# Kernel tuning notes

Hardware: AMD Instinct MI355X
Metric: run time of the kernel (lower is better)

The kernel has to match this reference:

```python
import jax, jax.numpy as jnp
import numpy as np

N = 100000      # num_nodes
E = 1600000     # num_edges (avg degree 16)
IN = 128        # in_channels
HID = 8         # hidden_channels (per head)
HEADS = 8
OUT = 64        # out_channels
NEG_SLOPE = 0.2


def setup_inputs() -> dict:
    key = jax.random.key(0)
    ks = jax.random.split(key, 11)
    s = 0.05
    return {
        "x": jax.random.normal(ks[0], (N, IN), jnp.float32),
        "edge_index": jax.random.randint(ks[1], (2, E), 0, N, dtype=jnp.int32),
        "W1": jax.random.normal(ks[2], (IN, HEADS * HID), jnp.float32) * s,
        "a_src1": jax.random.normal(ks[3], (HEADS, HID), jnp.float32) * s,
        "a_dst1": jax.random.normal(ks[4], (HEADS, HID), jnp.float32) * s,
        "b1": jnp.zeros((HEADS * HID,), jnp.float32),
        "W2": jax.random.normal(ks[5], (HEADS * HID, OUT), jnp.float32) * s,
        "a_src2": jax.random.normal(ks[6], (1, OUT), jnp.float32) * s,
        "a_dst2": jax.random.normal(ks[7], (1, OUT), jnp.float32) * s,
        "b2": jnp.zeros((OUT,), jnp.float32),
    }


def gat_conv(x, src, dst, W, a_src, a_dst, bias, heads, out_ch):
    """PyG GATConv (concat=True, dropout=0, self-loops already in src/dst)."""
    n = x.shape[0]
    h = (x @ W).reshape(n, heads, out_ch)               # [N, H, C]
    al_src = jnp.einsum('nhc,hc->nh', h, a_src)          # [N, H]
    al_dst = jnp.einsum('nhc,hc->nh', h, a_dst)          # [N, H]
    e = jax.nn.leaky_relu(al_src[src] + al_dst[dst], NEG_SLOPE)  # [E, H]
    # segment softmax over destination nodes (numerically stable)
    e_max = jax.ops.segment_max(e, dst, num_segments=n)  # [N, H]
    ex = jnp.exp(e - e_max[dst])
    denom = jax.ops.segment_sum(ex, dst, num_segments=n)
    alpha = ex / (denom[dst] + 1e-16)                    # [E, H]
    msg = h[src] * alpha[:, :, None]                     # [E, H, C]
    out = jax.ops.segment_sum(msg, dst, num_segments=n)  # [N, H, C]
    return out.reshape(n, heads * out_ch) + bias


def reference(x, edge_index, W1, a_src1, a_dst1, b1, W2, a_src2, a_dst2, b2):
    n = x.shape[0]
    loops = jnp.arange(n, dtype=edge_index.dtype)
    src = jnp.concatenate([edge_index[0], loops])        # add self-loops (PyG default)
    dst = jnp.concatenate([edge_index[1], loops])
    h = gat_conv(x, src, dst, W1, a_src1, a_dst1, b1, HEADS, HID)
    h = jax.nn.elu(h)
    out = gat_conv(h, src, dst, W2, a_src2, a_dst2, b2, 1, OUT)
    return out
```

## Files before the change

### kernel.cpp

```cpp
#include <hip/hip_runtime.h>
#include <hip/hip_bf16.h>

#define IN_CH   128
#define HEADS   8
#define HID     8
#define MID_CH  64
#define OUT_CH  64
#define CAP     64
#define NRANGE  8

typedef unsigned short u16;
__device__ __forceinline__ u16 f2bu(float f) {
    union { float f; unsigned int i; } v; v.f = f;
    unsigned int lsb = (v.i >> 16) & 1u;
    return (u16)((v.i + 0x7fffu + lsb) >> 16);
}
__device__ __forceinline__ float2 up2(unsigned int u) {
    union { unsigned int i; float f; } a, b;
    a.i = u << 16; b.i = u & 0xffff0000u;
    return make_float2(a.f, b.f);
}
__device__ __forceinline__ float lrelu(float e) { return (e > 0.f) ? e : 0.2f * e; }

#define FILL_ISSUE(U, D4, S4, P4)                                              \
    do {                                                                        \
        int range_ = (U) & (NRANGE - 1);                                        \
        int chunk_ = (U) >> 3;                                                  \
        int lo_ = (int)(((long long)N * range_) >> 3);                          \
        int hi_ = (int)(((long long)N * (range_ + 1)) >> 3);                    \
        int base_ = (chunk_ * 256 + threadIdx.x) * 4;                           \
        if (base_ + 3 < E) {                                                    \
            D4 = *(const int4*)(dst + base_);                                   \
            bool ix_ = (D4.x >= lo_ && D4.x < hi_);                             \
            bool iy_ = (D4.y >= lo_ && D4.y < hi_);                             \
            bool iz_ = (D4.z >= lo_ && D4.z < hi_);                             \
            bool iw_ = (D4.w >= lo_ && D4.w < hi_);                             \
            if (ix_ | iy_ | iz_ | iw_) {                                        \
                S4 = *(const int4*)(src + base_);                               \
                if (ix_) P4.x = atomicAdd(&deg[D4.x], 1);                       \
                if (iy_) P4.y = atomicAdd(&deg[D4.y], 1);                       \
                if (iz_) P4.z = atomicAdd(&deg[D4.z], 1);                       \
                if (iw_) P4.w = atomicAdd(&deg[D4.w], 1);                       \
            }                                                                   \
        } else {                                                                \
            for (int j_ = 0; j_ < 4; j_++) {                                    \
                int e_ = base_ + j_;                                            \
                if (e_ < E) {                                                   \
                    int d_ = dst[e_];                                           \
                    if (d_ >= lo_ && d_ < hi_) {                                \
                        int p_ = atomicAdd(&deg[d_], 1);                        \
                        if (p_ < CAP) adj[(size_t)d_ * CAP + p_] = src[e_];     \
                    }                                                           \
                }                                                               \
            }                                                                   \
        }                                                                       \
    } while (0)

#define FILL_STORE(D4, S4, P4)                                                  \
    do {                                                                        \
        if (P4.x < CAP) adj[(size_t)D4.x * CAP + P4.x] = S4.x;                  \
        if (P4.y < CAP) adj[(size_t)D4.y * CAP + P4.y] = S4.y;                  \
        if (P4.z < CAP) adj[(size_t)D4.z * CAP + P4.z] = S4.z;                  \
        if (P4.w < CAP) adj[(size_t)D4.w * CAP + P4.w] = S4.w;                  \
    } while (0)

__global__ __launch_bounds__(256, 4) void k12_fillgemm(
    const int* __restrict__ src, const int* __restrict__ dst,
    int* __restrict__ deg, int* __restrict__ adj,
    const float* __restrict__ x, const float* __restrict__ W1,
    const float* __restrict__ a_src, const float* __restrict__ a_dst,
    u16* __restrict__ h1b, float* __restrict__ als, float* __restrict__ ald,
    int E, int N, int grid, int nUnits)
{
    __shared__ float Wl[IN_CH * MID_CH];
    __shared__ float xl[16 * IN_CH];
    int tid = threadIdx.x;
    int bid = blockIdx.x;

    int4 dA = make_int4(0, 0, 0, 0), sA = make_int4(0, 0, 0, 0);
    int4 pA = make_int4(CAP, CAP, CAP, CAP);
    int4 dB = make_int4(0, 0, 0, 0), sB = make_int4(0, 0, 0, 0);
    int4 pB = make_int4(CAP, CAP, CAP, CAP);
    int uA = bid;
    int uB = bid + grid;
    if (uA < nUnits) FILL_ISSUE(uA, dA, sA, pA);
    if (uB < nUnits) FILL_ISSUE(uB, dB, sB, pB);

    {
        const float4* W4 = (const float4*)W1;
        float4* Wl4 = (float4*)Wl;
        #pragma unroll
        for (int i = tid; i < IN_CH * MID_CH / 4; i += 256) Wl4[i] = W4[i];
    }
    int base = bid * 16;
    {
        float4* xl4 = (float4*)xl;
        const float4* x4 = (const float4*)x;
        #pragma unroll
        for (int i = tid; i < 16 * IN_CH / 4; i += 256) {
            int r = i >> 5;
            int n = base + r;
            xl4[i] = (n < N) ? x4[(size_t)n * (IN_CH / 4) + (i & 31)]
                             : make_float4(0.f, 0.f, 0.f, 0.f);
        }
    }

    FILL_STORE(dA, sA, pA);
    FILL_STORE(dB, sB, pB);
    __syncthreads();

    int wave = tid >> 6, lane = tid & 63;
    int r0 = wave * 4;
    const float* xr0 = &xl[(r0 + 0) * IN_CH];
    const float* xr1 = &xl[(r0 + 1) * IN_CH];
    const float* xr2 = &xl[(r0 + 2) * IN_CH];
    const float* xr3 = &xl[(r0 + 3) * IN_CH];
    float acc0 = 0.f, acc1 = 0.f, acc2 = 0.f, acc3 = 0.f;
    #pragma unroll 8
    for (int kc = 0; kc < IN_CH; kc += 4) {
        float4 xa = *(const float4*)(xr0 + kc);
        float4 xb = *(const float4*)(xr1 + kc);
        float4 xc = *(const float4*)(xr2 + kc);
        float4 xd = *(const float4*)(xr3 + kc);
        float w0 = Wl[(kc + 0) * MID_CH + lane];
        float w1 = Wl[(kc + 1) * MID_CH + lane];
        float w2 = Wl[(kc + 2) * MID_CH + lane];
        float w3 = Wl[(kc + 3) * MID_CH + lane];
        acc0 = fmaf(xa.x, w0, acc0); acc0 = fmaf(xa.y, w1, acc0);
        acc0 = fmaf(xa.z, w2, acc0); acc0 = fmaf(xa.w, w3, acc0);
        acc1 = fmaf(xb.x, w0, acc1); acc1 = fmaf(xb.y, w1, acc1);
        acc1 = fmaf(xb.z, w2, acc1); acc1 = fmaf(xb.w, w3, acc1);
        acc2 = fmaf(xc.x, w0, acc2); acc2 = fmaf(xc.y, w1, acc2);
        acc2 = fmaf(xc.z, w2, acc2); acc2 = fmaf(xc.w, w3, acc2);
        acc3 = fmaf(xd.x, w0, acc3); acc3 = fmaf(xd.y, w1, acc3);
        acc3 = fmaf(xd.z, w2, acc3); acc3 = fmaf(xd.w, w3, acc3);
    }
    float accs[4] = {acc0, acc1, acc2, acc3};
    float asv = a_src[lane];
    float adv = a_dst[lane];
    #pragma unroll
    for (int g = 0; g < 4; g++) {
        int n = base + r0 + g;
        if (n >= N) continue;
        h1b[(size_t)n * MID_CH + lane] = f2bu(accs[g]);
        float vs = accs[g] * asv;
        float vd = accs[g] * adv;
        vs += __shfl_xor(vs, 1); vs += __shfl_xor(vs, 2); vs += __shfl_xor(vs, 4);
        vd += __shfl_xor(vd, 1); vd += __shfl_xor(vd, 2); vd += __shfl_xor(vd, 4);
        if ((lane & 7) == 0) {
            als[n * HEADS + (lane >> 3)] = vs;
            ald[n * HEADS + (lane >> 3)] = vd;
        }
    }
}

__global__ __launch_bounds__(256) void k3_agg1(
    const int* __restrict__ deg, const int* __restrict__ adj,
    const u16* __restrict__ h1b, const float* __restrict__ als,
    const float* __restrict__ ald, const float* __restrict__ b1,
    float* __restrict__ h2, int N)
{
    __shared__ int adjl[4][CAP];
    int wave = threadIdx.x >> 6, lane = threadIdx.x & 63;
    int n = blockIdx.x * 4 + wave;
    bool valid = (n < N);
    int nc = valid ? n : (N - 1);

    int g = lane >> 3;
    int c8 = lane & 7;
    int dg = deg[nc]; if (dg > CAP) dg = CAP;
    if (lane < dg) adjl[wave][lane] = adj[(size_t)nc * CAP + lane];
    float aldv = ald[nc * HEADS + c8];
    __syncthreads();

    const uint4* h1v = (const uint4*)h1b;
    float acc[8] = {0,0,0,0,0,0,0,0};
    float denom = 0.f;
    for (int i = g; i < dg; i += 8) {
        int s = adjl[wave][i];
        float ex = __expf(lrelu(als[s * HEADS + c8] + aldv));
        uint4 q = h1v[(size_t)s * 8 + c8];
        float2 p0 = up2(q.x), p1 = up2(q.y), p2 = up2(q.z), p3 = up2(q.w);
        denom += ex;
        acc[0] += ex * p0.x; acc[1] += ex * p0.y;
        acc[2] += ex * p1.x; acc[3] += ex * p1.y;
        acc[4] += ex * p2.x; acc[5] += ex * p2.y;
        acc[6] += ex * p3.x; acc[7] += ex * p3.y;
    }
    if (g == 0) {
        float ex = __expf(lrelu(als[nc * HEADS + c8] + aldv));
        uint4 q = h1v[(size_t)nc * 8 + c8];
        float2 p0 = up2(q.x), p1 = up2(q.y), p2 = up2(q.z), p3 = up2(q.w);
        denom += ex;
        acc[0] += ex * p0.x; acc[1] += ex * p0.y;
        acc[2] += ex * p1.x; acc[3] += ex * p1.y;
        acc[4] += ex * p2.x; acc[5] += ex * p2.y;
        acc[6] += ex * p3.x; acc[7] += ex * p3.y;
    }
    denom += __shfl_xor(denom, 8); denom += __shfl_xor(denom, 16); denom += __shfl_xor(denom, 32);
    #pragma unroll
    for (int j = 0; j < 8; j++) {
        acc[j] += __shfl_xor(acc[j], 8);
        acc[j] += __shfl_xor(acc[j], 16);
        acc[j] += __shfl_xor(acc[j], 32);
    }
    float inv = 1.f / (denom + 1e-16f);

    if (g == 0 && valid) {
        const float4* b4 = (const float4*)b1;
        float4 bl = b4[c8 * 2], bh = b4[c8 * 2 + 1];
        float4 o0, o1;
        o0.x = acc[0] * inv + bl.x; o0.y = acc[1] * inv + bl.y;
        o0.z = acc[2] * inv + bl.z; o0.w = acc[3] * inv + bl.w;
        o1.x = acc[4] * inv + bh.x; o1.y = acc[5] * inv + bh.y;
        o1.z = acc[6] * inv + bh.z; o1.w = acc[7] * inv + bh.w;
        o0.x = (o0.x > 0.f) ? o0.x : (__expf(o0.x) - 1.f);
        o0.y = (o0.y > 0.f) ? o0.y : (__expf(o0.y) - 1.f);
        o0.z = (o0.z > 0.f) ? o0.z : (__expf(o0.z) - 1.f);
        o0.w = (o0.w > 0.f) ? o0.w : (__expf(o0.w) - 1.f);
        o1.x = (o1.x > 0.f) ? o1.x : (__expf(o1.x) - 1.f);
        o1.y = (o1.y > 0.f) ? o1.y : (__expf(o1.y) - 1.f);
        o1.z = (o1.z > 0.f) ? o1.z : (__expf(o1.z) - 1.f);
        o1.w = (o1.w > 0.f) ? o1.w : (__expf(o1.w) - 1.f);
        float4* h2v = (float4*)h2;
        h2v[(size_t)n * 16 + c8 * 2]     = o0;
        h2v[(size_t)n * 16 + c8 * 2 + 1] = o1;
    }
}

__global__ __launch_bounds__(256) void k4_gemm2(
    const float* __restrict__ h2, const float* __restrict__ W2,
    const float* __restrict__ a_src, const float* __restrict__ a_dst,
    u16* __restrict__ t2b, float* __restrict__ als, float* __restrict__ ald, int N)
{
    __shared__ float Wl[MID_CH * OUT_CH];
    __shared__ float xl[16 * MID_CH];
    int tid = threadIdx.x;
    {
        const float4* W4 = (const float4*)W2;
        float4* Wl4 = (float4*)Wl;
        #pragma unroll
        for (int i = tid; i < MID_CH * OUT_CH / 4; i += 256) Wl4[i] = W4[i];
    }
    int base = blockIdx.x * 16;
    {
        float4* xl4 = (float4*)xl;
        const float4* x4 = (const float4*)h2;
        #pragma unroll
        for (int i = tid; i < 16 * MID_CH / 4; i += 256) {
            int r = i >> 4;
            int n = base + r;
            xl4[i] = (n < N) ? x4[(size_t)n * (MID_CH / 4) + (i & 15)]
                             : make_float4(0.f, 0.f, 0.f, 0.f);
        }
    }
    __syncthreads();

    int wave = tid >> 6, lane = tid & 63;
    int r0 = wave * 4;
    const float* xr0 = &xl[(r0 + 0) * MID_CH];
    const float* xr1 = &xl[(r0 + 1) * MID_CH];
    const float* xr2 = &xl[(r0 + 2) * MID_CH];
    const float* xr3 = &xl[(r0 + 3) * MID_CH];
    float acc0 = 0.f, acc1 = 0.f, acc2 = 0.f, acc3 = 0.f;
    #pragma unroll 8
    for (int kc = 0; kc < MID_CH; kc += 4) {
        float4 xa = *(const float4*)(xr0 + kc);
        float4 xb = *(const float4*)(xr1 + kc);
        float4 xc = *(const float4*)(xr2 + kc);
        float4 xd = *(const float4*)(xr3 + kc);
        float w0 = Wl[(kc + 0) * OUT_CH + lane];
        float w1 = Wl[(kc + 1) * OUT_CH + lane];
        float w2 = Wl[(kc + 2) * OUT_CH + lane];
        float w3 = Wl[(kc + 3) * OUT_CH + lane];
        acc0 = fmaf(xa.x, w0, acc0); acc0 = fmaf(xa.y, w1, acc0);
        acc0 = fmaf(xa.z, w2, acc0); acc0 = fmaf(xa.w, w3, acc0);
        acc1 = fmaf(xb.x, w0, acc1); acc1 = fmaf(xb.y, w1, acc1);
        acc1 = fmaf(xb.z, w2, acc1); acc1 = fmaf(xb.w, w3, acc1);
        acc2 = fmaf(xc.x, w0, acc2); acc2 = fmaf(xc.y, w1, acc2);
        acc2 = fmaf(xc.z, w2, acc2); acc2 = fmaf(xc.w, w3, acc2);
        acc3 = fmaf(xd.x, w0, acc3); acc3 = fmaf(xd.y, w1, acc3);
        acc3 = fmaf(xd.z, w2, acc3); acc3 = fmaf(xd.w, w3, acc3);
    }
    float accs[4] = {acc0, acc1, acc2, acc3};
    float asv = a_src[lane];
    float adv = a_dst[lane];
    #pragma unroll
    for (int g = 0; g < 4; g++) {
        int n = base + r0 + g;
        if (n >= N) continue;
        t2b[(size_t)n * OUT_CH + lane] = f2bu(accs[g]);
        float vs = accs[g] * asv;
        float vd = accs[g] * adv;
        #pragma unroll
        for (int off = 1; off < 64; off <<= 1) {
            vs += __shfl_xor(vs, off);
            vd += __shfl_xor(vd, off);
        }
        if (lane == 0) { als[n] = vs; ald[n] = vd; }
    }
}

__global__ __launch_bounds__(256) void k5_agg2(
    const int* __restrict__ deg, const int* __restrict__ adj,
    const u16* __restrict__ t2b, const float* __restrict__ als,
    const float* __restrict__ ald, const float* __restrict__ b2,
    float* __restrict__ out, int N)
{
    __shared__ int adjl[4][CAP];
    int wave = threadIdx.x >> 6, lane = threadIdx.x & 63;
    int n = blockIdx.x * 4 + wave;
    bool valid = (n < N);
    int nc = valid ? n : (N - 1);

    int g = lane >> 3;
    int c8 = lane & 7;
    int dg = deg[nc]; if (dg > CAP) dg = CAP;
    if (lane < dg) adjl[wave][lane] = adj[(size_t)nc * CAP + lane];
    float aldv = ald[nc];
    __syncthreads();

    const uint4* t2v = (const uint4*)t2b;
    float acc[8] = {0,0,0,0,0,0,0,0};
    float denom = 0.f;
    for (int i = g; i < dg; i += 8) {
        int s = adjl[wave][i];
        float ex = __expf(lrelu(als[s] + aldv));
        uint4 q = t2v[(size_t)s * 8 + c8];
        float2 p0 = up2(q.x), p1 = up2(q.y), p2 = up2(q.z), p3 = up2(q.w);
        denom += ex;
        acc[0] += ex * p0.x; acc[1] += ex * p0.y;
        acc[2] += ex * p1.x; acc[3] += ex * p1.y;
        acc[4] += ex * p2.x; acc[5] += ex * p2.y;
        acc[6] += ex * p3.x; acc[7] += ex * p3.y;
    }
    if (g == 0) {
        float ex = __expf(lrelu(als[nc] + aldv));
        uint4 q = t2v[(size_t)nc * 8 + c8];
        float2 p0 = up2(q.x), p1 = up2(q.y), p2 = up2(q.z), p3 = up2(q.w);
        denom += ex;
        acc[0] += ex * p0.x; acc[1] += ex * p0.y;
        acc[2] += ex * p1.x; acc[3] += ex * p1.y;
        acc[4] += ex * p2.x; acc[5] += ex * p2.y;
        acc[6] += ex * p3.x; acc[7] += ex * p3.y;
    }
    denom += __shfl_xor(denom, 8); denom += __shfl_xor(denom, 16); denom += __shfl_xor(denom, 32);
    #pragma unroll
    for (int j = 0; j < 8; j++) {
        acc[j] += __shfl_xor(acc[j], 8);
        acc[j] += __shfl_xor(acc[j], 16);
        acc[j] += __shfl_xor(acc[j], 32);
    }
    float inv = 1.f / (denom + 1e-16f);

    if (g == 0 && valid) {
        const float4* b4 = (const float4*)b2;
        float4 bl = b4[c8 * 2], bh = b4[c8 * 2 + 1];
        float4 o0, o1;
        o0.x = acc[0] * inv + bl.x; o0.y = acc[1] * inv + bl.y;
        o0.z = acc[2] * inv + bl.z; o0.w = acc[3] * inv + bl.w;
        o1.x = acc[4] * inv + bh.x; o1.y = acc[5] * inv + bh.y;
        o1.z = acc[6] * inv + bh.z; o1.w = acc[7] * inv + bh.w;
        float4* ov = (float4*)out;
        ov[(size_t)n * 16 + c8 * 2]     = o0;
        ov[(size_t)n * 16 + c8 * 2 + 1] = o1;
    }
}

extern "C" void kernel_launch(void* const* d_in, const int* in_sizes, int n_in,
                              void* d_out, int out_size, void* d_ws, size_t ws_size,
                              hipStream_t stream) {
    const float* x   = (const float*)d_in[0];
    const int*   ei  = (const int*)d_in[1];
    const float* W1  = (const float*)d_in[2];
    const float* as1 = (const float*)d_in[3];
    const float* ad1 = (const float*)d_in[4];
    const float* b1  = (const float*)d_in[5];
    const float* W2  = (const float*)d_in[6];
    const float* as2 = (const float*)d_in[7];
    const float* ad2 = (const float*)d_in[8];
    const float* b2  = (const float*)d_in[9];
    float* out = (float*)d_out;

    int N = in_sizes[0] / IN_CH;
    int E = in_sizes[1] / 2;
    const int* srcp = ei;
    const int* dstp = ei + E;

    char* w = (char*)d_ws;
    size_t off = 0;
    auto alloc = [&](size_t bytes) {
        void* p = w + off;
        off += (bytes + 255) & ~(size_t)255;
        return p;
    };
    int*   deg  = (int*)  alloc((size_t)N * 4);
    int*   adj  = (int*)  alloc((size_t)N * CAP * 4);
    u16*   h1b  = (u16*)  alloc((size_t)N * MID_CH * 2);
    float* als1 = (float*)alloc((size_t)N * HEADS * 4);
    float* ald1 = (float*)alloc((size_t)N * HEADS * 4);
    float* h2   = (float*)alloc((size_t)N * MID_CH * 4);
    u16*   t2b  = (u16*)  alloc((size_t)N * OUT_CH * 2);
    float* als2 = (float*)alloc((size_t)N * 4);
    float* ald2 = (float*)alloc((size_t)N * 4);
    (void)ws_size; (void)n_in; (void)out_size;

    hipMemsetAsync(deg, 0, (size_t)N * 4, stream);

    int chunks = (E + 1023) / 1024;
    int nUnits = chunks * NRANGE;
    int ngemm  = (N + 15) / 16;
    int grid   = ngemm;
    if (grid * 2 < nUnits) grid = (nUnits + 1) / 2;
    k12_fillgemm<<<grid, 256, 0, stream>>>(srcp, dstp, deg, adj,
                                           x, W1, as1, ad1, h1b, als1, ald1,
                                           E, N, grid, nUnits);
    k3_agg1<<<(N + 3) / 4, 256, 0, stream>>>(deg, adj, h1b, als1, ald1, b1, h2, N);
    k4_gemm2<<<(N + 15) / 16, 256, 0, stream>>>(h2, W2, as2, ad2, t2b, als2, ald2, N);
    k5_agg2<<<(N + 3) / 4, 256, 0, stream>>>(deg, adj, t2b, als2, ald2, b2, out, N);
}
```

Measured before the change: 363.1 us.

## Split fill/GEMM into role blocks and fuse layer-1 aggregation with GEMM2

The first kernel now gives its first 256 blocks the job of building the adjacency list in a strided loop, and the remaining blocks only run the layer-1 GEMM, where before every block did both jobs. Layer-1 aggregation is fused with the second GEMM: each wave writes its ELU output row to shared memory and multiplies it by W2 staged in LDS, so the fp32 h2 intermediate never goes to global memory and one launch is removed. The cost is that every aggregation block reloads the 16KB W2 into LDS plus an extra barrier. Each wave also computes only one output row in the GEMM, so there is less register reuse of W2 values.

After: 353.1 us. 2.7% less time.

```diff
diff --git a/kernel.cpp b/kernel.cpp
--- a/kernel.cpp
+++ b/kernel.cpp
@@ -8,6 +8,7 @@
 #define OUT_CH  64
 #define CAP     64
 #define NRANGE  8
+#define NFILLB  256
 
 typedef unsigned short u16;
 __device__ __forceinline__ u16 f2bu(float f) {
@@ -64,35 +65,48 @@
         if (P4.w < CAP) adj[(size_t)D4.w * CAP + P4.w] = S4.w;                  \
     } while (0)
 
-__global__ __launch_bounds__(256, 4) void k12_fillgemm(
+__global__ __launch_bounds__(256, 4) void k12_roles(
     const int* __restrict__ src, const int* __restrict__ dst,
     int* __restrict__ deg, int* __restrict__ adj,
     const float* __restrict__ x, const float* __restrict__ W1,
     const float* __restrict__ a_src, const float* __restrict__ a_dst,
     u16* __restrict__ h1b, float* __restrict__ als, float* __restrict__ ald,
-    int E, int N, int grid, int nUnits)
+    int E, int N)
 {
     __shared__ float Wl[IN_CH * MID_CH];
     __shared__ float xl[16 * IN_CH];
+    int bid = blockIdx.x;
     int tid = threadIdx.x;
-    int bid = blockIdx.x;
-
-    int4 dA = make_int4(0, 0, 0, 0), sA = make_int4(0, 0, 0, 0);
-    int4 pA = make_int4(CAP, CAP, CAP, CAP);
-    int4 dB = make_int4(0, 0, 0, 0), sB = make_int4(0, 0, 0, 0);
-    int4 pB = make_int4(CAP, CAP, CAP, CAP);
-    int uA = bid;
-    int uB = bid + grid;
-    if (uA < nUnits) FILL_ISSUE(uA, dA, sA, pA);
-    if (uB < nUnits) FILL_ISSUE(uB, dB, sB, pB);
-
+
+    if (bid < NFILLB) {
+        int range = bid & 7;
+        int cstart = bid >> 3;
+        int chunks = (E + 1023) >> 10;
+        for (int c = cstart; c < chunks; c += 64) {
+            int4 dA = make_int4(0,0,0,0), sA = make_int4(0,0,0,0);
+            int4 pA = make_int4(CAP,CAP,CAP,CAP);
+            int4 dB = make_int4(0,0,0,0), sB = make_int4(0,0,0,0);
+            int4 pB = make_int4(CAP,CAP,CAP,CAP);
+            int uA = c * 8 + range;
+            FILL_ISSUE(uA, dA, sA, pA);
+            if (c + 32 < chunks) {
+                int uB = (c + 32) * 8 + range;
+                FILL_ISSUE(uB, dB, sB, pB);
+            }
+            FILL_STORE(dA, sA, pA);
+            FILL_STORE(dB, sB, pB);
+        }
+        return;
+    }
+
+    int gid = bid - NFILLB;
     {
         const float4* W4 = (const float4*)W1;
         float4* Wl4 = (float4*)Wl;
         #pragma unroll
         for (int i = tid; i < IN_CH * MID_CH / 4; i += 256) Wl4[i] = W4[i];
     }
-    int base = bid * 16;
+    int base = gid * 16;
     {
         float4* xl4 = (float4*)xl;
         const float4* x4 = (const float4*)x;
@@ -104,9 +118,6 @@
                              : make_float4(0.f, 0.f, 0.f, 0.f);
         }
     }
-
-    FILL_STORE(dA, sA, pA);
-    FILL_STORE(dB, sB, pB);
     __syncthreads();
 
     int wave = tid >> 6, lane = tid & 63;
@@ -154,14 +165,26 @@
     }
 }
 
-__global__ __launch_bounds__(256) void k3_agg1(
+__global__ __launch_bounds__(256) void k34_agg1gemm2(
     const int* __restrict__ deg, const int* __restrict__ adj,
     const u16* __restrict__ h1b, const float* __restrict__ als,
     const float* __restrict__ ald, const float* __restrict__ b1,
-    float* __restrict__ h2, int N)
+    const float* __restrict__ W2, const float* __restrict__ as2,
+    const float* __restrict__ ad2,
+    u16* __restrict__ t2b, float* __restrict__ als2, float* __restrict__ ald2,
+    int N)
 {
+    __shared__ float W2l[MID_CH * OUT_CH];
     __shared__ int adjl[4][CAP];
-    int wave = threadIdx.x >> 6, lane = threadIdx.x & 63;
+    __shared__ float h2l[4][MID_CH];
+    int tid = threadIdx.x;
+    int wave = tid >> 6, lane = tid & 63;
+    {
+        const float4* W4 = (const float4*)W2;
+        float4* Wl4 = (float4*)W2l;
+        #pragma unroll
+        for (int i = tid; i < MID_CH * OUT_CH / 4; i += 256) Wl4[i] = W4[i];
+    }
     int n = blockIdx.x * 4 + wave;
     bool valid = (n < N);
     int nc = valid ? n : (N - 1);
@@ -222,82 +245,34 @@
         o1.y = (o1.y > 0.f) ? o1.y : (__expf(o1.y) - 1.f);
         o1.z = (o1.z > 0.f) ? o1.z : (__expf(o1.z) - 1.f);
         o1.w = (o1.w > 0.f) ? o1.w : (__expf(o1.w) - 1.f);
-        float4* h2v = (float4*)h2;
-        h2v[(size_t)n * 16 + c8 * 2]     = o0;
-        h2v[(size_t)n * 16 + c8 * 2 + 1] = o1;
-    }
-}
-
-__global__ __launch_bounds__(256) void k4_gemm2(
-    const float* __restrict__ h2, const float* __restrict__ W2,
-    const float* __restrict__ a_src, const float* __restrict__ a_dst,
-    u16* __restrict__ t2b, float* __restrict__ als, float* __restrict__ ald, int N)
-{
-    __shared__ float Wl[MID_CH * OUT_CH];
-    __shared__ float xl[16 * MID_CH];
-    int tid = threadIdx.x;
-    {
-        const float4* W4 = (const float4*)W2;
-        float4* Wl4 = (float4*)Wl;
-        #pragma unroll
-        for (int i = tid; i < MID_CH * OUT_CH / 4; i += 256) Wl4[i] = W4[i];
-    }
-    int base = blockIdx.x * 16;
-    {
-        float4* xl4 = (float4*)xl;
-        const float4* x4 = (const float4*)h2;
-        #pragma unroll
-        for (int i = tid; i < 16 * MID_CH / 4; i += 256) {
-            int r = i >> 4;
-            int n = base + r;
-            xl4[i] = (n < N) ? x4[(size_t)n * (MID_CH / 4) + (i & 15)]
-                             : make_float4(0.f, 0.f, 0.f, 0.f);
-        }
+        float4* h2v = (float4*)h2l[wave];
+        h2v[c8 * 2]     = o0;
+        h2v[c8 * 2 + 1] = o1;
     }
     __syncthreads();
 
-    int wave = tid >> 6, lane = tid & 63;
-    int r0 = wave * 4;
-    const float* xr0 = &xl[(r0 + 0) * MID_CH];
-    const float* xr1 = &xl[(r0 + 1) * MID_CH];
-    const float* xr2 = &xl[(r0 + 2) * MID_CH];
-    const float* xr3 = &xl[(r0 + 3) * MID_CH];
-    float acc0 = 0.f, acc1 = 0.f, acc2 = 0.f, acc3 = 0.f;
+    const float* hr = h2l[wave];
+    float acc2 = 0.f;
     #pragma unroll 8
     for (int kc = 0; kc < MID_CH; kc += 4) {
-        float4 xa = *(const float4*)(xr0 + kc);
-        float4 xb = *(const float4*)(xr1 + kc);
-        float4 xc = *(const float4*)(xr2 + kc);
-        float4 xd = *(const float4*)(xr3 + kc);
-        float w0 = Wl[(kc + 0) * OUT_CH + lane];
-        float w1 = Wl[(kc + 1) * OUT_CH + lane];
-        float w2 = Wl[(kc + 2) * OUT_CH + lane];
-        float w3 = Wl[(kc + 3) * OUT_CH + lane];
-        acc0 = fmaf(xa.x, w0, acc0); acc0 = fmaf(xa.y, w1, acc0);
-        acc0 = fmaf(xa.z, w2, acc0); acc0 = fmaf(xa.w, w3, acc0);
-        acc1 = fmaf(xb.x, w0, acc1); acc1 = fmaf(xb.y, w1, acc1);
-        acc1 = fmaf(xb.z, w2, acc1); acc1 = fmaf(xb.w, w3, acc1);
-        acc2 = fmaf(xc.x, w0, acc2); acc2 = fmaf(xc.y, w1, acc2);
-        acc2 = fmaf(xc.z, w2, acc2); acc2 = fmaf(xc.w, w3, acc2);
-        acc3 = fmaf(xd.x, w0, acc3); acc3 = fmaf(xd.y, w1, acc3);
-        acc3 = fmaf(xd.z, w2, acc3); acc3 = fmaf(xd.w, w3, acc3);
-    }
-    float accs[4] = {acc0, acc1, acc2, acc3};
-    float asv = a_src[lane];
-    float adv = a_dst[lane];
-    #pragma unroll
-    for (int g = 0; g < 4; g++) {
-        int n = base + r0 + g;
-        if (n >= N) continue;
-        t2b[(size_t)n * OUT_CH + lane] = f2bu(accs[g]);
-        float vs = accs[g] * asv;
-        float vd = accs[g] * adv;
+        float4 hv = *(const float4*)(hr + kc);
+        float w0 = W2l[(kc + 0) * OUT_CH + lane];
+        float w1 = W2l[(kc + 1) * OUT_CH + lane];
+        float w2 = W2l[(kc + 2) * OUT_CH + lane];
+        float w3 = W2l[(kc + 3) * OUT_CH + lane];
+        acc2 = fmaf(hv.x, w0, acc2); acc2 = fmaf(hv.y, w1, acc2);
+        acc2 = fmaf(hv.z, w2, acc2); acc2 = fmaf(hv.w, w3, acc2);
+    }
+    if (valid) {
+        t2b[(size_t)n * OUT_CH + lane] = f2bu(acc2);
+        float vs = acc2 * as2[lane];
+        float vd = acc2 * ad2[lane];
         #pragma unroll
         for (int off = 1; off < 64; off <<= 1) {
             vs += __shfl_xor(vs, off);
             vd += __shfl_xor(vd, off);
         }
-        if (lane == 0) { als[n] = vs; ald[n] = vd; }
+        if (lane == 0) { als2[n] = vs; ald2[n] = vd; }
     }
 }
 
@@ -399,7 +374,6 @@
     u16*   h1b  = (u16*)  alloc((size_t)N * MID_CH * 2);
     float* als1 = (float*)alloc((size_t)N * HEADS * 4);
     float* ald1 = (float*)alloc((size_t)N * HEADS * 4);
-    float* h2   = (float*)alloc((size_t)N * MID_CH * 4);
     u16*   t2b  = (u16*)  alloc((size_t)N * OUT_CH * 2);
     float* als2 = (float*)alloc((size_t)N * 4);
     float* ald2 = (float*)alloc((size_t)N * 4);
@@ -407,15 +381,11 @@
 
     hipMemsetAsync(deg, 0, (size_t)N * 4, stream);
 
-    int chunks = (E + 1023) / 1024;
-    int nUnits = chunks * NRANGE;
-    int ngemm  = (N + 15) / 16;
-    int grid   = ngemm;
-    if (grid * 2 < nUnits) grid = (nUnits + 1) / 2;
-    k12_fillgemm<<<grid, 256, 0, stream>>>(srcp, dstp, deg, adj,
-                                           x, W1, as1, ad1, h1b, als1, ald1,
-                                           E, N, grid, nUnits);
-    k3_agg1<<<(N + 3) / 4, 256, 0, stream>>>(deg, adj, h1b, als1, ald1, b1, h2, N);
-    k4_gemm2<<<(N + 15) / 16, 256, 0, stream>>>(h2, W2, as2, ad2, t2b, als2, ald2, N);
+    int ngemm = (N + 15) / 16;
+    k12_roles<<<NFILLB + ngemm, 256, 0, stream>>>(srcp, dstp, deg, adj,
+                                                  x, W1, as1, ad1, h1b, als1, ald1,
+                                                  E, N);
+    k34_agg1gemm2<<<(N + 3) / 4, 256, 0, stream>>>(deg, adj, h1b, als1, ald1, b1,
+                                                   W2, as2, ad2, t2b, als2, ald2, N);
     k5_agg2<<<(N + 3) / 4, 256, 0, stream>>>(deg, adj, t2b, als2, ald2, b2, out, N);
 }
```
